# Kernel tuning notes

Hardware: AMD Instinct MI355X
Metric: run time of the kernel (lower is better)

The kernel has to match this reference:

```python
import jax, jax.numpy as jnp
import numpy as np

B, N, D = 16, 4096, 64
LB_TH = 0.01
L2_LAMDA = 0.001
RECONS_LAMDA = 0.2


def _xavier(key, shape):
    fan_in, fan_out = shape[0], shape[1]
    a = float(np.sqrt(6.0 / (fan_in + fan_out)))
    return jax.random.uniform(key, shape, jnp.float32, -a, a)


def setup_inputs() -> dict:
    key = jax.random.key(0)
    k1, k2, k3 = jax.random.split(key, 3)
    X = jax.random.normal(k1, (B, N, D), jnp.float32)
    r_proj = _xavier(k2, (D, D))
    incidence_m = _xavier(k3, (N, N - 1))
    return {"X": X, "r_proj": r_proj, "incidence_m": incidence_m}


def reference(X, r_proj, incidence_m):
    n = incidence_m.shape[0]
    # clamp(min=lb_th) followed by masked_fill(~(v > lb_th), 0) == keep only orig > lb_th
    w = jnp.where(incidence_m > LB_TH, incidence_m, jnp.zeros((), X.dtype))  # [N, N-1]
    # scatter each row's N-1 weights into an NxN matrix, skipping the diagonal
    rows = jnp.arange(n)[:, None]                      # [N,1]
    cols = jnp.arange(n - 1)[None, :]                  # [1,N-1]
    full_cols = cols + (cols >= rows).astype(cols.dtype)  # [N,N-1]
    W = jnp.zeros((n, n), X.dtype).at[rows, full_cols].set(w)
    # per-node projection of master node features: X @ r_proj
    X_proj = jnp.einsum('bnd,de->bne', X, r_proj)      # [B,N,D]
    # neighbor reconstruction for every node at once
    recon = jnp.einsum('ij,bjd->bid', W, X)            # [B,N,D]
    recon_err = jnp.sqrt(jnp.sum((X_proj - recon) ** 2, axis=-1))  # [B,N]
    l1 = jnp.max(jnp.abs(w), axis=1)                   # [N] (max over single-row sum == max abs)
    l2 = jnp.sqrt(jnp.sum(w ** 2, axis=1))             # [N]
    recon_loss = recon_err * RECONS_LAMDA + l1[None, :] + L2_LAMDA * l2[None, :]
    incidence_all = W + jnp.eye(n, dtype=X.dtype)
    return recon_loss, incidence_all
```

## Files before the change

### kernel.cpp

```cpp
#include <hip/hip_runtime.h>
#include <hip/hip_bf16.h>

#define BB 16
#define NN 4096
#define DD 64
#define NM1 4095

typedef __bf16 bf16x8 __attribute__((ext_vector_type(8)));
typedef float f32x4 __attribute__((ext_vector_type(4)));

typedef __attribute__((address_space(1))) const void gas_void;
typedef __attribute__((address_space(3))) void las_void;


__global__ __launch_bounds__(256) void build_kernel(
    const float* __restrict__ inc, float* __restrict__ out_inc,
    __bf16* __restrict__ A16, float* __restrict__ mxa, float* __restrict__ ssa)
{
    int t = threadIdx.x;
    int base = blockIdx.x << 12;
    int rA = (int)((unsigned)base / NM1);
    float pm0 = 0.f, ps0 = 0.f, pm1 = 0.f, ps1 = 0.f;
    #pragma unroll
    for (int j = 0; j < 16; ++j) {
        int f = base + j * 256 + t;
        int i = (int)((unsigned)f / NM1);
        int c = f - i * NM1;
        float x = inc[f];
        float w = x > 0.01f ? x : 0.f;
        int dst = f + i + (c >= i);
        out_inc[dst] = w;
        A16[dst] = (__bf16)w;
        if (i == rA) { pm0 = fmaxf(pm0, w); ps0 += w * w; }
        else         { pm1 = fmaxf(pm1, w); ps1 += w * w; }
    }
    #pragma unroll
    for (int off = 32; off; off >>= 1) {
        pm0 = fmaxf(pm0, __shfl_down(pm0, off));
        ps0 += __shfl_down(ps0, off);
        pm1 = fmaxf(pm1, __shfl_down(pm1, off));
        ps1 += __shfl_down(ps1, off);
    }
    __shared__ float sm0[4], sq0[4], sm1[4], sq1[4];
    int wid = t >> 6;
    if ((t & 63) == 0) { sm0[wid] = pm0; sq0[wid] = ps0; sm1[wid] = pm1; sq1[wid] = ps1; }
    __syncthreads();
    if (t == 0) {
        float m0v = fmaxf(fmaxf(sm0[0], sm0[1]), fmaxf(sm0[2], sm0[3]));
        float s0v = sq0[0] + sq0[1] + sq0[2] + sq0[3];
        float m1v = fmaxf(fmaxf(sm1[0], sm1[1]), fmaxf(sm1[2], sm1[3]));
        float s1v = sq1[0] + sq1[1] + sq1[2] + sq1[3];
        atomicMax((unsigned*)(mxa + rA), __float_as_uint(m0v));
        atomicAdd(ssa + rA, s0v);
        int rB = rA + 1;
        if (rB < NN) {
            atomicMax((unsigned*)(mxa + rB), __float_as_uint(m1v));
            atomicAdd(ssa + rB, s1v);
        }
    }
}

__global__ __launch_bounds__(256) void xt_kernel(
    const float* __restrict__ X, __bf16* __restrict__ XT,
    float* __restrict__ out_inc, __bf16* __restrict__ A16)
{
    __shared__ __bf16 tile[64 * 72];
    int t = threadIdx.x;
    int ntile = blockIdx.x, b = blockIdx.y;
    int n = t >> 2, q = t & 3;
    const float* src = X + ((size_t)b * NN + ntile * 64 + n) * DD + q * 16;
    #pragma unroll
    for (int v = 0; v < 4; ++v) {
        f32x4 u = *(const f32x4*)(src + v * 4);
        #pragma unroll
        for (int j = 0; j < 4; ++j) {
            int d = q * 16 + v * 4 + j;
            tile[d * 72 + n] = (__bf16)u[j];
        }
    }
    __syncthreads();
    int d = t >> 2;
    __bf16* dst = XT + ((size_t)b * DD + d) * NN + ntile * 64 + q * 16;
    *(bf16x8*)dst       = *(bf16x8*)&tile[d * 72 + q * 16];
    *(bf16x8*)(dst + 8) = *(bf16x8*)&tile[d * 72 + q * 16 + 8];
    if (b == 0 && t < 64) {
        int r = ntile * 64 + t;
        out_inc[(size_t)r * NN + r] = 1.0f;
        A16[(size_t)r * NN + r] = (__bf16)1.0f;
    }
}

__global__ __launch_bounds__(256) void gemm_loss_kernel(
    const __bf16* __restrict__ A16, const __bf16* __restrict__ XT,
    const float* __restrict__ X, const float* __restrict__ rproj,
    const float* __restrict__ mxa, const float* __restrict__ ssa,
    float* __restrict__ loss)
{
    __shared__ __bf16 As[64 * 64];
    __shared__ __bf16 Xs[64 * 64];
    __shared__ float sred[64][2];

    int t = threadIdx.x;
    int wave = t >> 6, lane = t & 63;
    int quad = lane >> 4, ln = lane & 15;
    int m0 = blockIdx.x * 64;
    int b  = blockIdx.y;
    int mrow0 = (wave & 1) * 32;
    int ncol0 = (wave >> 1) * 32;
    int sr = lane >> 3;
    int so = lane & 7;

    const __bf16* Abase = A16 + (size_t)m0 * NN;
    const __bf16* Xbase = XT + (size_t)b * DD * NN;

    f32x4 acc[2][2];
    f32x4 zero = {0.f, 0.f, 0.f, 0.f};
    #pragma unroll
    for (int mt = 0; mt < 2; ++mt)
        #pragma unroll
        for (int nt = 0; nt < 2; ++nt) acc[mt][nt] = zero;

    for (int kt = 0; kt < NN / 64; ++kt) {
        int k0 = kt * 64;
        #pragma unroll
        for (int p = 0; p < 2; ++p) {
            int r0 = p * 32 + wave * 8;
            int r  = r0 + sr;
            int og = so ^ (r & 7);
            __builtin_amdgcn_global_load_lds(
                (gas_void*)(Abase + (size_t)r * NN + k0 + og * 8),
                (las_void*)(As + r0 * 64), 16, 0, 0);
            __builtin_amdgcn_global_load_lds(
                (gas_void*)(Xbase + (size_t)r * NN + k0 + og * 8),
                (las_void*)(Xs + r0 * 64), 16, 0, 0);
        }
        __syncthreads();
        #pragma unroll
        for (int kk = 0; kk < 64; kk += 32) {
            int oc = (kk >> 3) + quad;
            bf16x8 af[2], bfr[2];
            #pragma unroll
            for (int mt = 0; mt < 2; ++mt) {
                int r = mrow0 + mt * 16 + ln;
                af[mt] = *(const bf16x8*)&As[r * 64 + ((oc ^ (r & 7)) << 3)];
            }
            #pragma unroll
            for (int nt = 0; nt < 2; ++nt) {
                int n = ncol0 + nt * 16 + ln;
                bfr[nt] = *(const bf16x8*)&Xs[n * 64 + ((oc ^ (n & 7)) << 3)];
            }
            #pragma unroll
            for (int mt = 0; mt < 2; ++mt)
                #pragma unroll
                for (int nt = 0; nt < 2; ++nt)
                    acc[mt][nt] = __builtin_amdgcn_mfma_f32_16x16x32_bf16(
                        af[mt], bfr[nt], acc[mt][nt], 0, 0, 0);
        }
        __syncthreads();
    }

    {
        int rr = t >> 2, q = t & 3;
        const float* xs = X + ((size_t)b * NN + m0 + rr) * DD + q * 16;
        #pragma unroll
        for (int v = 0; v < 2; ++v) {
            f32x4 u0 = *(const f32x4*)(xs + v * 8);
            f32x4 u1 = *(const f32x4*)(xs + v * 8 + 4);
            bf16x8 w;
            #pragma unroll
            for (int j = 0; j < 4; ++j) { w[j] = (__bf16)u0[j]; w[j + 4] = (__bf16)u1[j]; }
            int o = (q * 2 + v) ^ (rr & 7);
            *(bf16x8*)&As[rr * 64 + o * 8] = w;
        }
        const float* rs = rproj + (size_t)rr * DD + q * 16;
        #pragma unroll
        for (int v = 0; v < 4; ++v) {
            f32x4 u = *(const f32x4*)(rs + v * 4);
            #pragma unroll
            for (int j = 0; j < 4; ++j) {
                int d = q * 16 + v * 4 + j;
                float val = u[j] + (d == rr ? 1.0f : 0.0f);
                Xs[d * 64 + (((rr >> 3) ^ (d & 7)) << 3) + (rr & 7)] = (__bf16)val;
            }
        }
    }
    __syncthreads();

    f32x4 xp[2][2];
    #pragma unroll
    for (int mt = 0; mt < 2; ++mt)
        #pragma unroll
        for (int nt = 0; nt < 2; ++nt) xp[mt][nt] = zero;
    #pragma unroll
    for (int kk = 0; kk < DD; kk += 32) {
        int oc = (kk >> 3) + quad;
        bf16x8 af[2], bfr[2];
        #pragma unroll
        for (int mt = 0; mt < 2; ++mt) {
            int r = mrow0 + mt * 16 + ln;
            af[mt] = *(const bf16x8*)&As[r * 64 + ((oc ^ (r & 7)) << 3)];
        }
        #pragma unroll
        for (int nt = 0; nt < 2; ++nt) {
            int n = ncol0 + nt * 16 + ln;
            bfr[nt] = *(const bf16x8*)&Xs[n * 64 + ((oc ^ (n & 7)) << 3)];
        }
        #pragma unroll
        for (int mt = 0; mt < 2; ++mt)
            #pragma unroll
            for (int nt = 0; nt < 2; ++nt)
                xp[mt][nt] = __builtin_amdgcn_mfma_f32_16x16x32_bf16(
                    af[mt], bfr[nt], xp[mt][nt], 0, 0, 0);
    }

    #pragma unroll
    for (int mt = 0; mt < 2; ++mt) {
        #pragma unroll
        for (int rg = 0; rg < 4; ++rg) {
            float s = 0.f;
            #pragma unroll
            for (int nt = 0; nt < 2; ++nt) {
                float df = xp[mt][nt][rg] - acc[mt][nt][rg];
                s += df * df;
            }
            s += __shfl_xor(s, 1);
            s += __shfl_xor(s, 2);
            s += __shfl_xor(s, 4);
            s += __shfl_xor(s, 8);
            if (ln == 0) sred[mrow0 + mt * 16 + quad * 4 + rg][wave >> 1] = s;
        }
    }
    __syncthreads();
    if (t < 64) {
        float s = sred[t][0] + sred[t][1];
        int row = m0 + t;
        loss[(size_t)b * NN + row] =
            0.2f * sqrtf(s) + mxa[row] + 0.001f * sqrtf(ssa[row]);
    }
}

extern "C" void kernel_launch(void* const* d_in, const int* in_sizes, int n_in,
                              void* d_out, int out_size, void* d_ws, size_t ws_size,
                              hipStream_t stream) {
    const float* X   = (const float*)d_in[0];
    const float* r   = (const float*)d_in[1];
    const float* inc = (const float*)d_in[2];
    float* out      = (float*)d_out;
    float* out_loss = out;
    float* out_inc  = out + (size_t)BB * NN;

    char* ws = (char*)d_ws;
    float*  mxa = (float*)ws;
    float*  ssa = (float*)(ws + 16384);
    __bf16* XT  = (__bf16*)(ws + 32768);
    __bf16* A16 = (__bf16*)(ws + 32768 + (size_t)8 * 1024 * 1024);

    hipMemsetAsync(mxa, 0, 32768, stream);

    hipLaunchKernelGGL(build_kernel, dim3(NM1), dim3(256), 0, stream,
                       inc, out_inc, A16, mxa, ssa);
    hipLaunchKernelGGL(xt_kernel, dim3(NN / 64, BB), dim3(256), 0, stream,
                       X, XT, out_inc, A16);
    hipLaunchKernelGGL(gemm_loss_kernel, dim3(NN / 64, BB), dim3(256), 0, stream,
                       A16, XT, X, r, mxa, ssa, out_loss);
}
```

Baseline: 195.8 us.

## Enlarge GEMM tile to 128 rows by two batches with triple-buffered async loads

The GEMM-loss kernel now has each 512-thread block handle 128 rows of the adjacency matrix for two batches, so every A tile loaded from global memory serves both batches. K-tiles are staged into a three-deep LDS ring using global_load_lds with explicit vmcnt waits, replacing the load-sync-compute-sync loop so memory traffic overlaps compute. The projection step accumulates directly into the negated GEMM result, and each wave writes its loss rows directly, which removes the cross-wave shared reduction. The cost is more LDS per block (96 KB), more accumulator registers and fewer blocks in the grid.

After: 190.8 us. -2.6%, faster.

```diff
diff --git a/kernel.cpp b/kernel.cpp
--- a/kernel.cpp
+++ b/kernel.cpp
@@ -90,127 +90,161 @@
     }
 }
 
-__global__ __launch_bounds__(256) void gemm_loss_kernel(
+__global__ __launch_bounds__(512, 2) void gemm_loss_kernel(
     const __bf16* __restrict__ A16, const __bf16* __restrict__ XT,
     const float* __restrict__ X, const float* __restrict__ rproj,
     const float* __restrict__ mxa, const float* __restrict__ ssa,
     float* __restrict__ loss)
 {
-    __shared__ __bf16 As[64 * 64];
-    __shared__ __bf16 Xs[64 * 64];
-    __shared__ float sred[64][2];
-
-    int t = threadIdx.x;
-    int wave = t >> 6, lane = t & 63;
-    int quad = lane >> 4, ln = lane & 15;
-    int m0 = blockIdx.x * 64;
-    int b  = blockIdx.y;
-    int mrow0 = (wave & 1) * 32;
-    int ncol0 = (wave >> 1) * 32;
-    int sr = lane >> 3;
-    int so = lane & 7;
+    __shared__ __bf16 smem[3 * 16384];
+
+    const int t = threadIdx.x;
+    const int wave = t >> 6, lane = t & 63;
+    const int quad = lane >> 4, ln = lane & 15;
+    const int sr = lane >> 3, so = lane & 7;
+    const int bq = wave >> 2;
+    const int wr = (wave & 3) << 5;
+    const int m0 = blockIdx.x * 128;
+    const int b0 = blockIdx.y * 2;
 
     const __bf16* Abase = A16 + (size_t)m0 * NN;
-    const __bf16* Xbase = XT + (size_t)b * DD * NN;
-
-    f32x4 acc[2][2];
+    const __bf16* XTb   = XT + (size_t)b0 * DD * NN;
+
+    f32x4 acc[2][4];
     f32x4 zero = {0.f, 0.f, 0.f, 0.f};
     #pragma unroll
     for (int mt = 0; mt < 2; ++mt)
         #pragma unroll
-        for (int nt = 0; nt < 2; ++nt) acc[mt][nt] = zero;
-
-    for (int kt = 0; kt < NN / 64; ++kt) {
-        int k0 = kt * 64;
+        for (int ct = 0; ct < 4; ++ct) acc[mt][ct] = zero;
+
+    auto stage = [&](int buf, int kt) {
+        __bf16* bA = smem + buf * 16384;
+        __bf16* bX = bA + 8192;
+        const int k0 = kt << 6;
         #pragma unroll
         for (int p = 0; p < 2; ++p) {
-            int r0 = p * 32 + wave * 8;
-            int r  = r0 + sr;
-            int og = so ^ (r & 7);
+            const int r0 = (p << 6) + (wave << 3);
+            const int r  = r0 + sr;
+            const int og = so ^ (r & 7);
             __builtin_amdgcn_global_load_lds(
-                (gas_void*)(Abase + (size_t)r * NN + k0 + og * 8),
-                (las_void*)(As + r0 * 64), 16, 0, 0);
+                (gas_void*)(Abase + (size_t)r * NN + k0 + (og << 3)),
+                (las_void*)(bA + r0 * 64), 16, 0, 0);
             __builtin_amdgcn_global_load_lds(
-                (gas_void*)(Xbase + (size_t)r * NN + k0 + og * 8),
-                (las_void*)(Xs + r0 * 64), 16, 0, 0);
-        }
-        __syncthreads();
+                (gas_void*)(XTb + (size_t)r * NN + k0 + (og << 3)),
+                (las_void*)(bX + r0 * 64), 16, 0, 0);
+        }
+    };
+
+    auto compute = [&](int buf) {
+        const __bf16* bA = smem + buf * 16384;
+        const __bf16* bX = bA + 8192 + (bq << 12);
         #pragma unroll
         for (int kk = 0; kk < 64; kk += 32) {
-            int oc = (kk >> 3) + quad;
-            bf16x8 af[2], bfr[2];
+            const int oc = (kk >> 3) + quad;
+            bf16x8 af[2], bfr[4];
             #pragma unroll
             for (int mt = 0; mt < 2; ++mt) {
-                int r = mrow0 + mt * 16 + ln;
-                af[mt] = *(const bf16x8*)&As[r * 64 + ((oc ^ (r & 7)) << 3)];
-            }
-            #pragma unroll
-            for (int nt = 0; nt < 2; ++nt) {
-                int n = ncol0 + nt * 16 + ln;
-                bfr[nt] = *(const bf16x8*)&Xs[n * 64 + ((oc ^ (n & 7)) << 3)];
+                const int r = wr + mt * 16 + ln;
+                af[mt] = *(const bf16x8*)&bA[r * 64 + ((oc ^ (r & 7)) << 3)];
+            }
+            #pragma unroll
+            for (int ct = 0; ct < 4; ++ct) {
+                const int n = ct * 16 + ln;
+                bfr[ct] = *(const bf16x8*)&bX[n * 64 + ((oc ^ (n & 7)) << 3)];
             }
             #pragma unroll
             for (int mt = 0; mt < 2; ++mt)
                 #pragma unroll
-                for (int nt = 0; nt < 2; ++nt)
-                    acc[mt][nt] = __builtin_amdgcn_mfma_f32_16x16x32_bf16(
-                        af[mt], bfr[nt], acc[mt][nt], 0, 0, 0);
-        }
-        __syncthreads();
+                for (int ct = 0; ct < 4; ++ct)
+                    acc[mt][ct] = __builtin_amdgcn_mfma_f32_16x16x32_bf16(
+                        af[mt], bfr[ct], acc[mt][ct], 0, 0, 0);
+        }
+    };
+
+    const int NT = NN / 64;
+    stage(0, 0);
+    stage(1, 1);
+    for (int kt = 0; kt < NT; ++kt) {
+        const int nx = kt + 2;
+        if (nx < NT) {
+            stage(nx % 3, nx);
+            asm volatile("s_waitcnt vmcnt(8)" ::: "memory");
+        } else if (kt == NT - 2) {
+            asm volatile("s_waitcnt vmcnt(4)" ::: "memory");
+        } else {
+            asm volatile("s_waitcnt vmcnt(0)" ::: "memory");
+        }
+        __builtin_amdgcn_s_barrier();
+        compute(kt % 3);
+        asm volatile("" ::: "memory");
+        __builtin_amdgcn_s_barrier();
     }
 
     {
-        int rr = t >> 2, q = t & 3;
-        const float* xs = X + ((size_t)b * NN + m0 + rr) * DD + q * 16;
-        #pragma unroll
-        for (int v = 0; v < 2; ++v) {
-            f32x4 u0 = *(const f32x4*)(xs + v * 8);
-            f32x4 u1 = *(const f32x4*)(xs + v * 8 + 4);
-            bf16x8 w;
-            #pragma unroll
-            for (int j = 0; j < 4; ++j) { w[j] = (__bf16)u0[j]; w[j + 4] = (__bf16)u1[j]; }
-            int o = (q * 2 + v) ^ (rr & 7);
-            *(bf16x8*)&As[rr * 64 + o * 8] = w;
-        }
-        const float* rs = rproj + (size_t)rr * DD + q * 16;
-        #pragma unroll
-        for (int v = 0; v < 4; ++v) {
-            f32x4 u = *(const f32x4*)(rs + v * 4);
-            #pragma unroll
-            for (int j = 0; j < 4; ++j) {
-                int d = q * 16 + v * 4 + j;
-                float val = u[j] + (d == rr ? 1.0f : 0.0f);
-                Xs[d * 64 + (((rr >> 3) ^ (d & 7)) << 3) + (rr & 7)] = (__bf16)val;
+        const int rr = t >> 2, q = t & 3;
+        #pragma unroll
+        for (int bb = 0; bb < 2; ++bb) {
+            const float* xs = X + ((size_t)(b0 + bb) * NN + m0 + rr) * DD + q * 16;
+            __bf16* XA = smem + bb * 8192;
+            #pragma unroll
+            for (int v = 0; v < 2; ++v) {
+                f32x4 u0 = *(const f32x4*)(xs + v * 8);
+                f32x4 u1 = *(const f32x4*)(xs + v * 8 + 4);
+                bf16x8 w;
+                #pragma unroll
+                for (int j = 0; j < 4; ++j) { w[j] = (__bf16)u0[j]; w[j + 4] = (__bf16)u1[j]; }
+                const int o = (q * 2 + v) ^ (rr & 7);
+                *(bf16x8*)&XA[rr * 64 + o * 8] = w;
+            }
+        }
+        if (t < 256) {
+            const int rr2 = t >> 2, q2 = t & 3;
+            const float* rs = rproj + (size_t)rr2 * DD + q2 * 16;
+            __bf16* R = smem + 16384;
+            #pragma unroll
+            for (int v = 0; v < 4; ++v) {
+                f32x4 u = *(const f32x4*)(rs + v * 4);
+                #pragma unroll
+                for (int j = 0; j < 4; ++j) {
+                    const int d = q2 * 16 + v * 4 + j;
+                    float val = u[j] + (d == rr2 ? 1.0f : 0.0f);
+                    R[d * 64 + (((rr2 >> 3) ^ (d & 7)) << 3) + (rr2 & 7)] = (__bf16)val;
+                }
             }
         }
     }
     __syncthreads();
 
-    f32x4 xp[2][2];
+    f32x4 dif[2][4];
     #pragma unroll
     for (int mt = 0; mt < 2; ++mt)
         #pragma unroll
-        for (int nt = 0; nt < 2; ++nt) xp[mt][nt] = zero;
-    #pragma unroll
-    for (int kk = 0; kk < DD; kk += 32) {
-        int oc = (kk >> 3) + quad;
-        bf16x8 af[2], bfr[2];
-        #pragma unroll
-        for (int mt = 0; mt < 2; ++mt) {
-            int r = mrow0 + mt * 16 + ln;
-            af[mt] = *(const bf16x8*)&As[r * 64 + ((oc ^ (r & 7)) << 3)];
-        }
-        #pragma unroll
-        for (int nt = 0; nt < 2; ++nt) {
-            int n = ncol0 + nt * 16 + ln;
-            bfr[nt] = *(const bf16x8*)&Xs[n * 64 + ((oc ^ (n & 7)) << 3)];
-        }
-        #pragma unroll
-        for (int mt = 0; mt < 2; ++mt)
-            #pragma unroll
-            for (int nt = 0; nt < 2; ++nt)
-                xp[mt][nt] = __builtin_amdgcn_mfma_f32_16x16x32_bf16(
-                    af[mt], bfr[nt], xp[mt][nt], 0, 0, 0);
+        for (int ct = 0; ct < 4; ++ct) dif[mt][ct] = -acc[mt][ct];
+
+    {
+        const __bf16* XA = smem + bq * 8192;
+        const __bf16* R  = smem + 16384;
+        #pragma unroll
+        for (int kk = 0; kk < DD; kk += 32) {
+            const int oc = (kk >> 3) + quad;
+            bf16x8 af[2], bfr[4];
+            #pragma unroll
+            for (int mt = 0; mt < 2; ++mt) {
+                const int r = wr + mt * 16 + ln;
+                af[mt] = *(const bf16x8*)&XA[r * 64 + ((oc ^ (r & 7)) << 3)];
+            }
+            #pragma unroll
+            for (int ct = 0; ct < 4; ++ct) {
+                const int n = ct * 16 + ln;
+                bfr[ct] = *(const bf16x8*)&R[n * 64 + ((oc ^ (n & 7)) << 3)];
+            }
+            #pragma unroll
+            for (int mt = 0; mt < 2; ++mt)
+                #pragma unroll
+                for (int ct = 0; ct < 4; ++ct)
+                    dif[mt][ct] = __builtin_amdgcn_mfma_f32_16x16x32_bf16(
+                        af[mt], bfr[ct], dif[mt][ct], 0, 0, 0);
+        }
     }
 
     #pragma unroll
@@ -219,23 +253,20 @@
         for (int rg = 0; rg < 4; ++rg) {
             float s = 0.f;
             #pragma unroll
-            for (int nt = 0; nt < 2; ++nt) {
-                float df = xp[mt][nt][rg] - acc[mt][nt][rg];
-                s += df * df;
+            for (int ct = 0; ct < 4; ++ct) {
+                float d = dif[mt][ct][rg];
+                s += d * d;
             }
             s += __shfl_xor(s, 1);
             s += __shfl_xor(s, 2);
             s += __shfl_xor(s, 4);
             s += __shfl_xor(s, 8);
-            if (ln == 0) sred[mrow0 + mt * 16 + quad * 4 + rg][wave >> 1] = s;
-        }
-    }
-    __syncthreads();
-    if (t < 64) {
-        float s = sred[t][0] + sred[t][1];
-        int row = m0 + t;
-        loss[(size_t)b * NN + row] =
-            0.2f * sqrtf(s) + mxa[row] + 0.001f * sqrtf(ssa[row]);
+            if (ln == 0) {
+                int row = m0 + wr + mt * 16 + quad * 4 + rg;
+                loss[(size_t)(b0 + bq) * NN + row] =
+                    0.2f * sqrtf(s) + mxa[row] + 0.001f * sqrtf(ssa[row]);
+            }
+        }
     }
 }
 
@@ -261,6 +292,6 @@
                        inc, out_inc, A16, mxa, ssa);
     hipLaunchKernelGGL(xt_kernel, dim3(NN / 64, BB), dim3(256), 0, stream,
                        X, XT, out_inc, A16);
-    hipLaunchKernelGGL(gemm_loss_kernel, dim3(NN / 64, BB), dim3(256), 0, stream,
+    hipLaunchKernelGGL(gemm_loss_kernel, dim3(NN / 128, BB / 2), dim3(512), 0, stream,
                        A16, XT, X, r, mxa, ssa, out_loss);
 }
```
